# Optimization experiments

Measured on AMD Instinct MI355X. Metric: run time of the kernel, lower is better.

## Reference

```python
import jax, jax.numpy as jnp
import numpy as np

N, E, G, H, D = 50000, 800000, 64, 2, 128  # nodes, edges, graphs, heads, out_channels
NEG_SLOPE_ATT = 0.2   # GATv2 default negative_slope
NEG_SLOPE_OUT = 0.01  # torch.nn.LeakyReLU default
BN_EPS = 1e-5


def setup_inputs() -> dict:
    key = jax.random.key(0)
    ks = jax.random.split(key, 12)
    x = jax.random.normal(ks[0], (N, 1), jnp.float32)
    edge_index = jax.random.randint(ks[1], (2, E), 0, N, dtype=jnp.int64)
    edge_attr = jax.random.normal(ks[2], (E,), jnp.float32)
    batch = jnp.sort(jax.random.randint(ks[3], (N,), 0, G, dtype=jnp.int64))
    # GATv2Conv params: lin_l/lin_r: Linear(1, H*D) with bias; lin_edge: Linear(1, H*D) no bias
    Wl = jax.random.normal(ks[4], (1, H * D), jnp.float32) * 0.5
    bl = jax.random.normal(ks[5], (H * D,), jnp.float32) * 0.1
    Wr = jax.random.normal(ks[6], (1, H * D), jnp.float32) * 0.5
    br = jax.random.normal(ks[7], (H * D,), jnp.float32) * 0.1
    We = jax.random.normal(ks[8], (1, H * D), jnp.float32) * 0.5
    att = jax.random.normal(ks[9], (H, D), jnp.float32) * 0.5
    bias = jax.random.normal(ks[10], (D,), jnp.float32) * 0.1
    gamma = jnp.ones((D,), jnp.float32)
    beta = jnp.zeros((D,), jnp.float32)
    return {"x": x, "edge_index": edge_index, "edge_attr": edge_attr, "batch": batch,
            "Wl": Wl, "bl": bl, "Wr": Wr, "br": br, "We": We, "att": att,
            "bias": bias, "gamma": gamma, "beta": beta}


def reference(x, edge_index, edge_attr, batch, Wl, bl, Wr, br, We, att, bias, gamma, beta):
    n = x.shape[0]
    src, dst = edge_index[0], edge_index[1]  # message flows src -> dst
    # node transforms: [N, H, D]
    xl = (x @ Wl + bl).reshape(n, H, D)  # lin_l (source side, also the message value)
    xr = (x @ Wr + br).reshape(n, H, D)  # lin_r (destination side)
    # edge feature embedding: [E, H, D]
    ee = (edge_attr[:, None] @ We).reshape(-1, H, D)
    # GATv2 scoring: leaky_relu(x_j + x_i + e), then dot with attention vector
    m = jax.nn.leaky_relu(xl[src] + xr[dst] + ee, NEG_SLOPE_ATT)  # [E, H, D]
    alpha = jnp.einsum('ehd,hd->eh', m, att)  # [E, H]
    # scatter-softmax over incoming edges per destination node
    amax = jax.ops.segment_max(alpha, dst, num_segments=n)  # [N, H]
    ea = jnp.exp(alpha - amax[dst])
    denom = jax.ops.segment_sum(ea, dst, num_segments=n)
    alpha = ea / (denom[dst] + 1e-16)
    # weighted scatter-add aggregation of x_j
    out = jax.ops.segment_sum(xl[src] * alpha[..., None], dst, num_segments=n)  # [N, H, D]
    out = out.mean(axis=1) + bias  # concat=False -> head average, then conv bias
    # BatchNorm1d in training mode (biased variance over nodes)
    mean = out.mean(axis=0)
    var = ((out - mean) ** 2).mean(axis=0)
    out = (out - mean) * jax.lax.rsqrt(var + BN_EPS) * gamma + beta
    out = jax.nn.leaky_relu(out, NEG_SLOPE_OUT)
    # graph-level scatter_add pooling
    return jax.ops.segment_sum(out, batch, num_segments=G)  # [G, D]
```

## Files before the change

### kernel.cpp

```cpp
#include <hip/hip_runtime.h>
#include <math.h>

#define NN 50000
#define NE 800000
#define NG 64

#define WS_C     0
#define WS_ACC   16
#define WS_BNSUM (WS_ACC + 4*NN)
#define WS_BNSQ  (WS_BNSUM + 128)
#define WS_HEAD  (WS_BNSQ + 128)
#define WS_PREV  (WS_HEAD + 4*NN)
#define WS_STAGE (WS_PREV + NE)
#define WS_END   (WS_STAGE + 4*NE)
#define WS_NEED_BYTES ((size_t)WS_END * 4 + 256)

#define LEND 0xFFFFFFFFu

static_assert(((WS_STAGE * 4) % 16) == 0, "stage 16B alignment");
static_assert(NE % 4 == 0, "edge unroll");

extern "C" __global__ __launch_bounds__(256)
void k0_init(float* __restrict__ ws,
             const float* __restrict__ att, const float* __restrict__ Wl,
             const float* __restrict__ Wr, const float* __restrict__ We,
             const float* __restrict__ bl, const float* __restrict__ br,
             float* __restrict__ out, int dense)
{
  int tid = blockIdx.x * 256 + threadIdx.x;
  int nt = gridDim.x * 256;
  if (dense) {
    unsigned* head = (unsigned*)(ws + WS_HEAD);
    for (int i = tid; i < 4 * NN; i += nt) head[i] = LEND;
  } else {
    for (int i = tid; i < 4 * NN; i += nt) ws[WS_ACC + i] = 0.f;
  }
  for (int i = tid; i < 256; i += nt) ws[WS_BNSUM + i] = 0.f;
  for (int i = tid; i < NG * 128; i += nt) out[i] = 0.f;
  if (blockIdx.x == 0) {
    __shared__ float red[4][256];
    int t = threadIdx.x;
    float a = att[t];
    red[0][t] = a * Wl[t];
    red[1][t] = a * Wr[t];
    red[2][t] = a * We[t];
    red[3][t] = a * (bl[t] + br[t]);
    __syncthreads();
    if (t < 8) {
      int k = t >> 1, h = t & 1;
      float s = 0.f;
      for (int d = 0; d < 128; ++d) s += red[k][h * 128 + d];
      ws[WS_C + h * 4 + k] = s;
    }
  }
}

#define STEP(wl_, wr_, we_, bb_, at_, xs_, xd_, ae_, acc_)                 \
  { float tt = fmaf(we_, ae_, bb_); tt = fmaf(wr_, xd_, tt);               \
    tt = fmaf(wl_, xs_, tt); acc_ = fmaf(fabsf(tt), at_, acc_); }

#define STEP4(c, q0, q1, q2, q3)                                           \
  STEP(wl.c, wr.c, we.c, bb.c, at.c, xs0, xd0, ae0, q0)                    \
  STEP(wl.c, wr.c, we.c, bb.c, at.c, xs1, xd1, ae1, q1)                    \
  STEP(wl.c, wr.c, we.c, bb.c, at.c, xs2, xd2, ae2, q2)                    \
  STEP(wl.c, wr.c, we.c, bb.c, at.c, xs3, xd3, ae3, q3)

#define SCORE_CORE                                                         \
  int4 s4 = *(const int4*)&ei[base];                                       \
  int4 dd4 = *(const int4*)&ei[NE + base];                                 \
  float4 ae4 = *(const float4*)&eattr[base];                               \
  float xs0 = x[s4.x], xs1 = x[s4.y], xs2 = x[s4.z], xs3 = x[s4.w];        \
  float xd0 = x[dd4.x], xd1 = x[dd4.y], xd2 = x[dd4.z], xd3 = x[dd4.w];    \
  float ae0 = ae4.x, ae1 = ae4.y, ae2 = ae4.z, ae3 = ae4.w;

#define SCORE_LOOPS                                                        \
  float a00 = 0.f, a01 = 0.f, a02 = 0.f, a03 = 0.f;                        \
  float a10 = 0.f, a11 = 0.f, a12 = 0.f, a13 = 0.f;                        \
  _Pragma("unroll 2")                                                      \
  for (int j = 0; j < 128; j += 4) {                                       \
    float4 wl = *(const float4*)&sWl[j];                                   \
    float4 wr = *(const float4*)&sWr[j];                                   \
    float4 we = *(const float4*)&sWe[j];                                   \
    float4 bb = *(const float4*)&sB[j];                                    \
    float4 at = *(const float4*)&sAt[j];                                   \
    STEP4(x, a00, a01, a02, a03)                                           \
    STEP4(y, a00, a01, a02, a03)                                           \
    STEP4(z, a00, a01, a02, a03)                                           \
    STEP4(w, a00, a01, a02, a03)                                           \
  }                                                                        \
  _Pragma("unroll 2")                                                      \
  for (int j = 128; j < 256; j += 4) {                                     \
    float4 wl = *(const float4*)&sWl[j];                                   \
    float4 wr = *(const float4*)&sWr[j];                                   \
    float4 we = *(const float4*)&sWe[j];                                   \
    float4 bb = *(const float4*)&sB[j];                                    \
    float4 at = *(const float4*)&sAt[j];                                   \
    STEP4(x, a10, a11, a12, a13)                                           \
    STEP4(y, a10, a11, a12, a13)                                           \
    STEP4(z, a10, a11, a12, a13)                                           \
    STEP4(w, a10, a11, a12, a13)                                           \
  }                                                                        \
  float4 c0 = *(const float4*)&ws[WS_C];                                   \
  float4 c1 = *(const float4*)&ws[WS_C + 4];

#define SMEM_WEIGHTS                                                       \
  __shared__ __align__(16) float sWl[256], sWr[256], sWe[256], sB[256], sAt[256]; \
  { int t = threadIdx.x;                                                   \
    sWl[t] = Wl[t]; sWr[t] = Wr[t]; sWe[t] = We[t];                        \
    sB[t] = bl[t] + br[t]; sAt[t] = att[t]; }                              \
  __syncthreads();

#define SCORES(xs_, xd_, ae_, accA, accB, out0, out1)                      \
  { float lin0 = fmaf(c0.x, xs_, fmaf(c0.y, xd_, fmaf(c0.z, ae_, c0.w))); \
    out0 = fmaf(0.4f, accA, 0.6f * lin0);                                  \
    float lin1 = fmaf(c1.x, xs_, fmaf(c1.y, xd_, fmaf(c1.z, ae_, c1.w))); \
    out1 = fmaf(0.4f, accB, 0.6f * lin1); }

extern "C" __global__ __launch_bounds__(256)
void ke_edge(const int* __restrict__ ei, const float* __restrict__ x,
             const float* __restrict__ eattr,
             const float* __restrict__ Wl, const float* __restrict__ Wr,
             const float* __restrict__ We, const float* __restrict__ bl,
             const float* __restrict__ br, const float* __restrict__ att,
             float* __restrict__ ws)
{
  SMEM_WEIGHTS
  int base = (blockIdx.x * 256 + threadIdx.x) * 4;
  if (base >= NE) return;
  SCORE_CORE
  unsigned* head = (unsigned*)(ws + WS_HEAD);
  unsigned pv0 = atomicExch(&head[4 * dd4.x + 0], (unsigned)(base + 0));
  unsigned pv1 = atomicExch(&head[4 * dd4.y + 1], (unsigned)(base + 1));
  unsigned pv2 = atomicExch(&head[4 * dd4.z + 2], (unsigned)(base + 2));
  unsigned pv3 = atomicExch(&head[4 * dd4.w + 3], (unsigned)(base + 3));
  SCORE_LOOPS
  float4* stage = (float4*)(ws + WS_STAGE);
  unsigned* prev = (unsigned*)(ws + WS_PREV);
  float s0, s1;
  float4 pay0, pay1, pay2, pay3;
#define PAY(xs_, xd_, ae_, accA, accB, pp)                                 \
  { SCORES(xs_, xd_, ae_, accA, accB, s0, s1)                              \
    float e0 = __expf(s0), e1 = __expf(s1);                                \
    pp = make_float4(e0, e1, e0 * xs_, e1 * xs_); }
  PAY(xs0, xd0, ae0, a00, a10, pay0)
  PAY(xs1, xd1, ae1, a01, a11, pay1)
  PAY(xs2, xd2, ae2, a02, a12, pay2)
  PAY(xs3, xd3, ae3, a03, a13, pay3)
#undef PAY
  stage[base + 0] = pay0;
  stage[base + 1] = pay1;
  stage[base + 2] = pay2;
  stage[base + 3] = pay3;
  *(uint4*)&prev[base] = make_uint4(pv0, pv1, pv2, pv3);
}

extern "C" __global__ __launch_bounds__(256)
void kf_gather(float* __restrict__ ws)
{
  int n = blockIdx.x * 256 + threadIdx.x;
  if (n >= NN) return;
  const unsigned* head = (const unsigned*)(ws + WS_HEAD);
  const unsigned* prev = (const unsigned*)(ws + WS_PREV);
  const float4* stage = (const float4*)(ws + WS_STAGE);
  uint4 p = *(const uint4*)&head[4 * n];
  float4 A0 = make_float4(0.f, 0.f, 0.f, 0.f);
  float4 A1 = A0, A2 = A0, A3 = A0;
  while ((p.x & p.y & p.z & p.w) != LEND) {
#define HOP(pc, Ac)                                                        \
    if (pc != LEND) {                                                      \
      float4 q = stage[pc];                                                \
      unsigned np = prev[pc];                                              \
      Ac.x += q.x; Ac.y += q.y; Ac.z += q.z; Ac.w += q.w;                  \
      pc = np;                                                             \
    }
    HOP(p.x, A0) HOP(p.y, A1) HOP(p.z, A2) HOP(p.w, A3)
#undef HOP
  }
  float4 r;
  r.x = (A0.x + A1.x) + (A2.x + A3.x);
  r.y = (A0.y + A1.y) + (A2.y + A3.y);
  r.z = (A0.z + A1.z) + (A2.z + A3.z);
  r.w = (A0.w + A1.w) + (A2.w + A3.w);
  *(float4*)&ws[WS_ACC + 4 * n] = r;
}

extern "C" __global__ __launch_bounds__(256)
void k12f(const int* __restrict__ ei, const float* __restrict__ x,
          const float* __restrict__ eattr,
          const float* __restrict__ Wl, const float* __restrict__ Wr,
          const float* __restrict__ We, const float* __restrict__ bl,
          const float* __restrict__ br, const float* __restrict__ att,
          float* __restrict__ ws)
{
  SMEM_WEIGHTS
  int base = (blockIdx.x * 256 + threadIdx.x) * 4;
  if (base >= NE) return;
  SCORE_CORE
  SCORE_LOOPS
  float* acc = ws + WS_ACC;
  float s0, s1;
#define EPI2(xs_, xd_, ae_, accA, accB, dsti)                              \
  { SCORES(xs_, xd_, ae_, accA, accB, s0, s1)                              \
    float e0 = __expf(s0), e1 = __expf(s1);                                \
    float* a = &acc[4 * dsti];                                             \
    atomicAdd(a + 0, e0); atomicAdd(a + 1, e1);                            \
    atomicAdd(a + 2, e0 * xs_); atomicAdd(a + 3, e1 * xs_); }
  EPI2(xs0, xd0, ae0, a00, a10, dd4.x)
  EPI2(xs1, xd1, ae1, a01, a11, dd4.y)
  EPI2(xs2, xd2, ae2, a02, a12, dd4.z)
  EPI2(xs3, xd3, ae3, a03, a13, dd4.w)
#undef EPI2
}

__device__ __forceinline__ float node_out4(float4 a, float wl0, float wl1,
                                           float b0, float b1, float bs)
{
  float r0 = 1.f / (a.x + 1e-16f);
  float r1 = 1.f / (a.y + 1e-16f);
  return 0.5f * (fmaf(wl0, a.z * r0, b0 * (a.x * r0)) +
                 fmaf(wl1, a.w * r1, b1 * (a.y * r1))) + bs;
}

extern "C" __global__ __launch_bounds__(256)
void k3_stats(const float* __restrict__ Wl, const float* __restrict__ bl,
              const float* __restrict__ bias, float* __restrict__ ws)
{
  int d = threadIdx.x & 127;
  int row = threadIdx.x >> 7;
  float wl0 = Wl[d], wl1 = Wl[128 + d];
  float b0 = bl[d], b1 = bl[128 + d];
  float bs = bias[d];
  float sum = 0.f, sq = 0.f;
  for (int n = blockIdx.x * 2 + row; n < NN; n += gridDim.x * 2) {
    float4 a = *(const float4*)&ws[WS_ACC + 4 * n];
    float o = node_out4(a, wl0, wl1, b0, b1, bs);
    sum += o;
    sq = fmaf(o, o, sq);
  }
  __shared__ float l1[256], l2[256];
  l1[threadIdx.x] = sum; l2[threadIdx.x] = sq;
  __syncthreads();
  if (row == 0) {
    atomicAdd(&ws[WS_BNSUM + d], l1[d] + l1[128 + d]);
    atomicAdd(&ws[WS_BNSQ + d], l2[d] + l2[128 + d]);
  }
}

extern "C" __global__ __launch_bounds__(256)
void k4_pool(const int* __restrict__ batch,
             const float* __restrict__ Wl, const float* __restrict__ bl,
             const float* __restrict__ bias, const float* __restrict__ gamma,
             const float* __restrict__ beta,
             float* __restrict__ ws, float* __restrict__ out)
{
  const int CHUNK = (NN + (int)gridDim.x - 1) / (int)gridDim.x;
  int n0 = blockIdx.x * CHUNK;
  if (n0 >= NN) return;
  int n1 = n0 + CHUNK; if (n1 > NN) n1 = NN;
  int d = threadIdx.x & 127;
  int row = threadIdx.x >> 7;
  const float invN = 1.f / (float)NN;
  float mean = ws[WS_BNSUM + d] * invN;
  float var = fmaf(ws[WS_BNSQ + d], invN, -mean * mean);
  float scale = gamma[d] * rsqrtf(var + 1e-5f);
  float shift = fmaf(-mean, scale, beta[d]);
  float wl0 = Wl[d], wl1 = Wl[128 + d];
  float b0 = bl[d], b1 = bl[128 + d];
  float bs = bias[d];
  __shared__ float pool[4][128];
  for (int i = threadIdx.x; i < 512; i += 256) ((float*)pool)[i] = 0.f;
  __syncthreads();
  int g0 = batch[n0];
  for (int n = n0 + row; n < n1; n += 2) {
    float4 a = *(const float4*)&ws[WS_ACC + 4 * n];
    float o = node_out4(a, wl0, wl1, b0, b1, bs);
    float v = fmaf(o, scale, shift);
    v = v > 0.f ? v : 0.01f * v;
    int g = batch[n];
    int slot = g - g0;
    if (slot < 4) atomicAdd(&pool[slot][d], v);
    else atomicAdd(&out[g * 128 + d], v);
  }
  __syncthreads();
  for (int i = threadIdx.x; i < 512; i += 256) {
    int slot = i >> 7, dd = i & 127;
    int g = g0 + slot;
    float v = pool[slot][dd];
    if (g < NG && v != 0.f) atomicAdd(&out[g * 128 + dd], v);
  }
}

extern "C" void kernel_launch(void* const* d_in, const int* in_sizes, int n_in,
                              void* d_out, int out_size, void* d_ws, size_t ws_size,
                              hipStream_t stream) {
  const float* x     = (const float*)d_in[0];
  const int*   ei    = (const int*)d_in[1];
  const float* eattr = (const float*)d_in[2];
  const int*   batch = (const int*)d_in[3];
  const float* Wl    = (const float*)d_in[4];
  const float* bl    = (const float*)d_in[5];
  const float* Wr    = (const float*)d_in[6];
  const float* br    = (const float*)d_in[7];
  const float* We    = (const float*)d_in[8];
  const float* att   = (const float*)d_in[9];
  const float* bias  = (const float*)d_in[10];
  const float* gam   = (const float*)d_in[11];
  const float* bet   = (const float*)d_in[12];
  float* ws  = (float*)d_ws;
  float* out = (float*)d_out;

  const bool dense = (ws_size >= WS_NEED_BYTES);
  const int EB = (NE / 4 + 255) / 256;

  hipLaunchKernelGGL(k0_init, dim3(128), dim3(256), 0, stream,
                     ws, att, Wl, Wr, We, bl, br, out, dense ? 1 : 0);
  if (dense) {
    hipLaunchKernelGGL(ke_edge, dim3(EB), dim3(256), 0, stream,
                       ei, x, eattr, Wl, Wr, We, bl, br, att, ws);
    hipLaunchKernelGGL(kf_gather, dim3((NN + 255) / 256), dim3(256), 0, stream, ws);
  } else {
    hipLaunchKernelGGL(k12f, dim3(EB), dim3(256), 0, stream,
                       ei, x, eattr, Wl, Wr, We, bl, br, att, ws);
  }
  hipLaunchKernelGGL(k3_stats, dim3(256), dim3(256), 0, stream,
                     Wl, bl, bias, ws);
  hipLaunchKernelGGL(k4_pool, dim3(256), dim3(256), 0, stream,
                     batch, Wl, bl, bias, gam, bet, ws, out);
}
```

Before: 229.5 us.

## Fuse all stages into one cooperative persistent kernel with grid syncs

New measurement: 574.8 us. +150.5%, slower.

```diff
diff --git a/kernel.cpp b/kernel.cpp
--- a/kernel.cpp
+++ b/kernel.cpp
@@ -1,5 +1,8 @@
 #include <hip/hip_runtime.h>
+#include <hip/hip_cooperative_groups.h>
 #include <math.h>
+
+namespace cg = cooperative_groups;
 
 #define NN 50000
 #define NE 800000
@@ -9,6 +12,7 @@
 #define WS_ACC   16
 #define WS_BNSUM (WS_ACC + 4*NN)
 #define WS_BNSQ  (WS_BNSUM + 128)
+#define WS_MOM   WS_BNSUM
 #define WS_HEAD  (WS_BNSQ + 128)
 #define WS_PREV  (WS_HEAD + 4*NN)
 #define WS_STAGE (WS_PREV + NE)
@@ -16,44 +20,10 @@
 #define WS_NEED_BYTES ((size_t)WS_END * 4 + 256)
 
 #define LEND 0xFFFFFFFFu
+#define NQ (NE / 4)
 
 static_assert(((WS_STAGE * 4) % 16) == 0, "stage 16B alignment");
 static_assert(NE % 4 == 0, "edge unroll");
-
-extern "C" __global__ __launch_bounds__(256)
-void k0_init(float* __restrict__ ws,
-             const float* __restrict__ att, const float* __restrict__ Wl,
-             const float* __restrict__ Wr, const float* __restrict__ We,
-             const float* __restrict__ bl, const float* __restrict__ br,
-             float* __restrict__ out, int dense)
-{
-  int tid = blockIdx.x * 256 + threadIdx.x;
-  int nt = gridDim.x * 256;
-  if (dense) {
-    unsigned* head = (unsigned*)(ws + WS_HEAD);
-    for (int i = tid; i < 4 * NN; i += nt) head[i] = LEND;
-  } else {
-    for (int i = tid; i < 4 * NN; i += nt) ws[WS_ACC + i] = 0.f;
-  }
-  for (int i = tid; i < 256; i += nt) ws[WS_BNSUM + i] = 0.f;
-  for (int i = tid; i < NG * 128; i += nt) out[i] = 0.f;
-  if (blockIdx.x == 0) {
-    __shared__ float red[4][256];
-    int t = threadIdx.x;
-    float a = att[t];
-    red[0][t] = a * Wl[t];
-    red[1][t] = a * Wr[t];
-    red[2][t] = a * We[t];
-    red[3][t] = a * (bl[t] + br[t]);
-    __syncthreads();
-    if (t < 8) {
-      int k = t >> 1, h = t & 1;
-      float s = 0.f;
-      for (int d = 0; d < 128; ++d) s += red[k][h * 128 + d];
-      ws[WS_C + h * 4 + k] = s;
-    }
-  }
-}
 
 #define STEP(wl_, wr_, we_, bb_, at_, xs_, xd_, ae_, acc_)                 \
   { float tt = fmaf(we_, ae_, bb_); tt = fmaf(wr_, xd_, tt);               \
@@ -103,8 +73,10 @@
   float4 c0 = *(const float4*)&ws[WS_C];                                   \
   float4 c1 = *(const float4*)&ws[WS_C + 4];
 
-#define SMEM_WEIGHTS                                                       \
-  __shared__ __align__(16) float sWl[256], sWr[256], sWe[256], sB[256], sAt[256]; \
+#define SMEM_WEIGHTS_DECL                                                  \
+  __shared__ __align__(16) float sWl[256], sWr[256], sWe[256], sB[256], sAt[256];
+
+#define SMEM_WEIGHTS_LOAD                                                  \
   { int t = threadIdx.x;                                                   \
     sWl[t] = Wl[t]; sWr[t] = Wr[t]; sWe[t] = We[t];                        \
     sB[t] = bl[t] + br[t]; sAt[t] = att[t]; }                              \
@@ -115,6 +87,222 @@
     out0 = fmaf(0.4f, accA, 0.6f * lin0);                                  \
     float lin1 = fmaf(c1.x, xs_, fmaf(c1.y, xd_, fmaf(c1.z, ae_, c1.w))); \
     out1 = fmaf(0.4f, accB, 0.6f * lin1); }
+
+extern "C" __global__ __launch_bounds__(256, 4)
+void kmega(const int* __restrict__ ei, const float* __restrict__ x,
+           const float* __restrict__ eattr, const int* __restrict__ batch,
+           const float* __restrict__ Wl, const float* __restrict__ bl,
+           const float* __restrict__ Wr, const float* __restrict__ br,
+           const float* __restrict__ We, const float* __restrict__ att,
+           const float* __restrict__ bias, const float* __restrict__ gamma,
+           const float* __restrict__ beta,
+           float* __restrict__ ws, float* __restrict__ out)
+{
+  cg::grid_group grid = cg::this_grid();
+  SMEM_WEIGHTS_DECL
+  __shared__ float red[4][256];
+  __shared__ float smom[56];
+  __shared__ float pool[4][128];
+  SMEM_WEIGHTS_LOAD
+
+  const int t = threadIdx.x;
+  const int gtid = blockIdx.x * 256 + t;
+  const int gsz = gridDim.x * 256;
+
+  {
+    unsigned* head = (unsigned*)(ws + WS_HEAD);
+    for (int i = gtid; i < 4 * NN; i += gsz) head[i] = LEND;
+    for (int i = gtid; i < 14; i += gsz) ws[WS_MOM + i] = 0.f;
+    for (int i = gtid; i < NG * 128; i += gsz) out[i] = 0.f;
+    if (blockIdx.x == 0) {
+      float a = sAt[t];
+      red[0][t] = a * sWl[t];
+      red[1][t] = a * sWr[t];
+      red[2][t] = a * sWe[t];
+      red[3][t] = a * sB[t];
+      __syncthreads();
+      if (t < 8) {
+        int k = t >> 1, h = t & 1;
+        float s = 0.f;
+        for (int d = 0; d < 128; ++d) s += red[k][h * 128 + d];
+        ws[WS_C + h * 4 + k] = s;
+      }
+    }
+  }
+  grid.sync();
+
+  {
+    unsigned* head = (unsigned*)(ws + WS_HEAD);
+    float4* stage = (float4*)(ws + WS_STAGE);
+    unsigned* prev = (unsigned*)(ws + WS_PREV);
+    for (int q = gtid; q < NQ; q += gsz) {
+      int base = q * 4;
+      SCORE_CORE
+      unsigned pv0 = atomicExch(&head[4 * dd4.x + 0], (unsigned)(base + 0));
+      unsigned pv1 = atomicExch(&head[4 * dd4.y + 1], (unsigned)(base + 1));
+      unsigned pv2 = atomicExch(&head[4 * dd4.z + 2], (unsigned)(base + 2));
+      unsigned pv3 = atomicExch(&head[4 * dd4.w + 3], (unsigned)(base + 3));
+      SCORE_LOOPS
+      float s0, s1;
+      float4 pay0, pay1, pay2, pay3;
+#define PAY(xs_, xd_, ae_, accA, accB, pp)                                 \
+      { SCORES(xs_, xd_, ae_, accA, accB, s0, s1)                          \
+        float e0 = __expf(s0), e1 = __expf(s1);                            \
+        pp = make_float4(e0, e1, e0 * xs_, e1 * xs_); }
+      PAY(xs0, xd0, ae0, a00, a10, pay0)
+      PAY(xs1, xd1, ae1, a01, a11, pay1)
+      PAY(xs2, xd2, ae2, a02, a12, pay2)
+      PAY(xs3, xd3, ae3, a03, a13, pay3)
+#undef PAY
+      stage[base + 0] = pay0;
+      stage[base + 1] = pay1;
+      stage[base + 2] = pay2;
+      stage[base + 3] = pay3;
+      *(uint4*)&prev[base] = make_uint4(pv0, pv1, pv2, pv3);
+    }
+  }
+  grid.sync();
+
+  {
+    const unsigned* head = (const unsigned*)(ws + WS_HEAD);
+    const unsigned* prev = (const unsigned*)(ws + WS_PREV);
+    const float4* stage = (const float4*)(ws + WS_STAGE);
+    float f1 = 0.f, f2 = 0.f, f3 = 0.f, f4 = 0.f;
+    for (int n = gtid; n < NN; n += gsz) {
+      uint4 p = *(const uint4*)&head[4 * n];
+      float4 A0 = make_float4(0.f, 0.f, 0.f, 0.f);
+      float4 A1 = A0, A2 = A0, A3 = A0;
+      while ((p.x & p.y & p.z & p.w) != LEND) {
+#define HOP(pc, Ac)                                                        \
+        if (pc != LEND) {                                                  \
+          float4 qq = stage[pc];                                           \
+          unsigned np = prev[pc];                                          \
+          Ac.x += qq.x; Ac.y += qq.y; Ac.z += qq.z; Ac.w += qq.w;          \
+          pc = np;                                                         \
+        }
+        HOP(p.x, A0) HOP(p.y, A1) HOP(p.z, A2) HOP(p.w, A3)
+#undef HOP
+      }
+      float den0 = (A0.x + A1.x) + (A2.x + A3.x);
+      float den1 = (A0.y + A1.y) + (A2.y + A3.y);
+      float t10  = (A0.z + A1.z) + (A2.z + A3.z);
+      float t11  = (A0.w + A1.w) + (A2.w + A3.w);
+      *(float4*)&ws[WS_ACC + 4 * n] = make_float4(den0, den1, t10, t11);
+      float r0 = 1.f / (den0 + 1e-16f);
+      float r1 = 1.f / (den1 + 1e-16f);
+      f1 += den0 * r0; f2 += t10 * r0; f3 += den1 * r1; f4 += t11 * r1;
+    }
+    float pm[14] = { f1, f2, f3, f4,
+                     f1*f1, f1*f2, f1*f3, f1*f4,
+                     f2*f2, f2*f3, f2*f4,
+                     f3*f3, f3*f4, f4*f4 };
+#pragma unroll
+    for (int k = 0; k < 14; ++k) {
+      float v = pm[k];
+#pragma unroll
+      for (int m = 32; m >= 1; m >>= 1) v += __shfl_xor(v, m);
+      pm[k] = v;
+    }
+    int wid = t >> 6, lane = t & 63;
+    if (lane == 0) {
+#pragma unroll
+      for (int k = 0; k < 14; ++k) smom[wid * 14 + k] = pm[k];
+    }
+    __syncthreads();
+    if (t < 14) {
+      float s = smom[t] + smom[14 + t] + smom[28 + t] + smom[42 + t];
+      if (s != 0.f) atomicAdd(&ws[WS_MOM + t], s);
+    }
+  }
+  grid.sync();
+
+  {
+    const int CHUNK = (NN + (int)gridDim.x - 1) / (int)gridDim.x;
+    int n0 = blockIdx.x * CHUNK;
+    if (n0 < NN) {
+      int n1 = n0 + CHUNK; if (n1 > NN) n1 = NN;
+      int d = t & 127;
+      int row = t >> 7;
+      float S1 = ws[WS_MOM + 0], S2 = ws[WS_MOM + 1];
+      float S3 = ws[WS_MOM + 2], S4 = ws[WS_MOM + 3];
+      float M11 = ws[WS_MOM + 4], M12 = ws[WS_MOM + 5], M13 = ws[WS_MOM + 6];
+      float M14 = ws[WS_MOM + 7], M22 = ws[WS_MOM + 8], M23 = ws[WS_MOM + 9];
+      float M24 = ws[WS_MOM + 10], M33 = ws[WS_MOM + 11], M34 = ws[WS_MOM + 12];
+      float M44 = ws[WS_MOM + 13];
+      float g1 = 0.5f * bl[d], g2 = 0.5f * Wl[d];
+      float g3 = 0.5f * bl[128 + d], g4 = 0.5f * Wl[128 + d];
+      float g5 = bias[d];
+      const float invN = 1.f / (float)NN;
+      float dotS = g1 * S1 + g2 * S2 + g3 * S3 + g4 * S4;
+      float mean = (dotS + (float)NN * g5) * invN;
+      float sumsq = g1*g1*M11 + g2*g2*M22 + g3*g3*M33 + g4*g4*M44
+                  + 2.f*(g1*g2*M12 + g1*g3*M13 + g1*g4*M14
+                       + g2*g3*M23 + g2*g4*M24 + g3*g4*M34)
+                  + 2.f*g5*dotS + (float)NN*g5*g5;
+      float var = fmaf(sumsq, invN, -mean * mean);
+      float scale = gamma[d] * rsqrtf(var + 1e-5f);
+      float shift = fmaf(-mean, scale, beta[d]);
+      for (int i = t; i < 512; i += 256) ((float*)pool)[i] = 0.f;
+      __syncthreads();
+      int g0 = batch[n0];
+      for (int n = n0 + row; n < n1; n += 2) {
+        float4 a = *(const float4*)&ws[WS_ACC + 4 * n];
+        float r0 = 1.f / (a.x + 1e-16f);
+        float r1 = 1.f / (a.y + 1e-16f);
+        float o = g1 * (a.x * r0) + g2 * (a.z * r0)
+                + g3 * (a.y * r1) + g4 * (a.w * r1) + g5;
+        float v = fmaf(o, scale, shift);
+        v = v > 0.f ? v : 0.01f * v;
+        int g = batch[n];
+        int slot = g - g0;
+        if (slot < 4) atomicAdd(&pool[slot][d], v);
+        else atomicAdd(&out[g * 128 + d], v);
+      }
+      __syncthreads();
+      for (int i = t; i < 512; i += 256) {
+        int slot = i >> 7, dd = i & 127;
+        int g = g0 + slot;
+        float v = pool[slot][dd];
+        if (g < NG && v != 0.f) atomicAdd(&out[g * 128 + dd], v);
+      }
+    }
+  }
+}
+
+extern "C" __global__ __launch_bounds__(256)
+void k0_init(float* __restrict__ ws,
+             const float* __restrict__ att, const float* __restrict__ Wl,
+             const float* __restrict__ Wr, const float* __restrict__ We,
+             const float* __restrict__ bl, const float* __restrict__ br,
+             float* __restrict__ out, int dense)
+{
+  int tid = blockIdx.x * 256 + threadIdx.x;
+  int nt = gridDim.x * 256;
+  if (dense) {
+    unsigned* head = (unsigned*)(ws + WS_HEAD);
+    for (int i = tid; i < 4 * NN; i += nt) head[i] = LEND;
+  } else {
+    for (int i = tid; i < 4 * NN; i += nt) ws[WS_ACC + i] = 0.f;
+  }
+  for (int i = tid; i < 256; i += nt) ws[WS_BNSUM + i] = 0.f;
+  for (int i = tid; i < NG * 128; i += nt) out[i] = 0.f;
+  if (blockIdx.x == 0) {
+    __shared__ float red[4][256];
+    int t = threadIdx.x;
+    float a = att[t];
+    red[0][t] = a * Wl[t];
+    red[1][t] = a * Wr[t];
+    red[2][t] = a * We[t];
+    red[3][t] = a * (bl[t] + br[t]);
+    __syncthreads();
+    if (t < 8) {
+      int k = t >> 1, h = t & 1;
+      float s = 0.f;
+      for (int d = 0; d < 128; ++d) s += red[k][h * 128 + d];
+      ws[WS_C + h * 4 + k] = s;
+    }
+  }
+}
 
 extern "C" __global__ __launch_bounds__(256)
 void ke_edge(const int* __restrict__ ei, const float* __restrict__ x,
@@ -124,7 +312,8 @@
              const float* __restrict__ br, const float* __restrict__ att,
              float* __restrict__ ws)
 {
-  SMEM_WEIGHTS
+  SMEM_WEIGHTS_DECL
+  SMEM_WEIGHTS_LOAD
   int base = (blockIdx.x * 256 + threadIdx.x) * 4;
   if (base >= NE) return;
   SCORE_CORE
@@ -192,7 +381,8 @@
           const float* __restrict__ br, const float* __restrict__ att,
           float* __restrict__ ws)
 {
-  SMEM_WEIGHTS
+  SMEM_WEIGHTS_DECL
+  SMEM_WEIGHTS_LOAD
   int base = (blockIdx.x * 256 + threadIdx.x) * 4;
   if (base >= NE) return;
   SCORE_CORE
@@ -312,18 +502,32 @@
   const bool dense = (ws_size >= WS_NEED_BYTES);
   const int EB = (NE / 4 + 255) / 256;
 
-  hipLaunchKernelGGL(k0_init, dim3(128), dim3(256), 0, stream,
-                     ws, att, Wl, Wr, We, bl, br, out, dense ? 1 : 0);
+  bool done = false;
   if (dense) {
-    hipLaunchKernelGGL(ke_edge, dim3(EB), dim3(256), 0, stream,
-                       ei, x, eattr, Wl, Wr, We, bl, br, att, ws);
-    hipLaunchKernelGGL(kf_gather, dim3((NN + 255) / 256), dim3(256), 0, stream, ws);
-  } else {
-    hipLaunchKernelGGL(k12f, dim3(EB), dim3(256), 0, stream,
-                       ei, x, eattr, Wl, Wr, We, bl, br, att, ws);
-  }
-  hipLaunchKernelGGL(k3_stats, dim3(256), dim3(256), 0, stream,
-                     Wl, bl, bias, ws);
-  hipLaunchKernelGGL(k4_pool, dim3(256), dim3(256), 0, stream,
-                     batch, Wl, bl, bias, gam, bet, ws, out);
-}
+    void* kargs[] = { (void*)&ei, (void*)&x, (void*)&eattr, (void*)&batch,
+                      (void*)&Wl, (void*)&bl, (void*)&Wr, (void*)&br,
+                      (void*)&We, (void*)&att, (void*)&bias, (void*)&gam,
+                      (void*)&bet, (void*)&ws, (void*)&out };
+    hipError_t e = hipLaunchCooperativeKernel((const void*)kmega,
+                                              dim3(1024), dim3(256),
+                                              kargs, 0, stream);
+    if (e == hipSuccess) done = true;
+    else (void)hipGetLastError();
+  }
+  if (!done) {
+    hipLaunchKernelGGL(k0_init, dim3(128), dim3(256), 0, stream,
+                       ws, att, Wl, Wr, We, bl, br, out, dense ? 1 : 0);
+    if (dense) {
+      hipLaunchKernelGGL(ke_edge, dim3(EB), dim3(256), 0, stream,
+                         ei, x, eattr, Wl, Wr, We, bl, br, att, ws);
+      hipLaunchKernelGGL(kf_gather, dim3((NN + 255) / 256), dim3(256), 0, stream, ws);
+    } else {
+      hipLaunchKernelGGL(k12f, dim3(EB), dim3(256), 0, stream,
+                         ei, x, eattr, Wl, Wr, We, bl, br, att, ws);
+    }
+    hipLaunchKernelGGL(k3_stats, dim3(256), dim3(256), 0, stream,
+                       Wl, bl, bias, ws);
+    hipLaunchKernelGGL(k4_pool, dim3(256), dim3(256), 0, stream,
+                       batch, Wl, bl, bias, gam, bet, ws, out);
+  }
+}
```

## Fold BatchNorm statistics into gather via per-node moment sums, drop stats pass

Applied to the files above, without the earlier changes.

Result: slower. 373.2 us (+62.7%).

```diff
diff --git a/kernel.cpp b/kernel.cpp
--- a/kernel.cpp
+++ b/kernel.cpp
@@ -9,6 +9,7 @@
 #define WS_ACC   16
 #define WS_BNSUM (WS_ACC + 4*NN)
 #define WS_BNSQ  (WS_BNSUM + 128)
+#define WS_MOM   WS_BNSUM
 #define WS_HEAD  (WS_BNSQ + 128)
 #define WS_PREV  (WS_HEAD + 4*NN)
 #define WS_STAGE (WS_PREV + NE)
@@ -19,41 +20,6 @@
 
 static_assert(((WS_STAGE * 4) % 16) == 0, "stage 16B alignment");
 static_assert(NE % 4 == 0, "edge unroll");
-
-extern "C" __global__ __launch_bounds__(256)
-void k0_init(float* __restrict__ ws,
-             const float* __restrict__ att, const float* __restrict__ Wl,
-             const float* __restrict__ Wr, const float* __restrict__ We,
-             const float* __restrict__ bl, const float* __restrict__ br,
-             float* __restrict__ out, int dense)
-{
-  int tid = blockIdx.x * 256 + threadIdx.x;
-  int nt = gridDim.x * 256;
-  if (dense) {
-    unsigned* head = (unsigned*)(ws + WS_HEAD);
-    for (int i = tid; i < 4 * NN; i += nt) head[i] = LEND;
-  } else {
-    for (int i = tid; i < 4 * NN; i += nt) ws[WS_ACC + i] = 0.f;
-  }
-  for (int i = tid; i < 256; i += nt) ws[WS_BNSUM + i] = 0.f;
-  for (int i = tid; i < NG * 128; i += nt) out[i] = 0.f;
-  if (blockIdx.x == 0) {
-    __shared__ float red[4][256];
-    int t = threadIdx.x;
-    float a = att[t];
-    red[0][t] = a * Wl[t];
-    red[1][t] = a * Wr[t];
-    red[2][t] = a * We[t];
-    red[3][t] = a * (bl[t] + br[t]);
-    __syncthreads();
-    if (t < 8) {
-      int k = t >> 1, h = t & 1;
-      float s = 0.f;
-      for (int d = 0; d < 128; ++d) s += red[k][h * 128 + d];
-      ws[WS_C + h * 4 + k] = s;
-    }
-  }
-}
 
 #define STEP(wl_, wr_, we_, bb_, at_, xs_, xd_, ae_, acc_)                 \
   { float tt = fmaf(we_, ae_, bb_); tt = fmaf(wr_, xd_, tt);               \
@@ -103,8 +69,10 @@
   float4 c0 = *(const float4*)&ws[WS_C];                                   \
   float4 c1 = *(const float4*)&ws[WS_C + 4];
 
-#define SMEM_WEIGHTS                                                       \
-  __shared__ __align__(16) float sWl[256], sWr[256], sWe[256], sB[256], sAt[256]; \
+#define SMEM_WEIGHTS_DECL                                                  \
+  __shared__ __align__(16) float sWl[256], sWr[256], sWe[256], sB[256], sAt[256];
+
+#define SMEM_WEIGHTS_LOAD                                                  \
   { int t = threadIdx.x;                                                   \
     sWl[t] = Wl[t]; sWr[t] = Wr[t]; sWe[t] = We[t];                        \
     sB[t] = bl[t] + br[t]; sAt[t] = att[t]; }                              \
@@ -115,6 +83,42 @@
     out0 = fmaf(0.4f, accA, 0.6f * lin0);                                  \
     float lin1 = fmaf(c1.x, xs_, fmaf(c1.y, xd_, fmaf(c1.z, ae_, c1.w))); \
     out1 = fmaf(0.4f, accB, 0.6f * lin1); }
+
+extern "C" __global__ __launch_bounds__(256)
+void k0_init(float* __restrict__ ws,
+             const float* __restrict__ att, const float* __restrict__ Wl,
+             const float* __restrict__ Wr, const float* __restrict__ We,
+             const float* __restrict__ bl, const float* __restrict__ br,
+             float* __restrict__ out, int dense)
+{
+  int tid = blockIdx.x * 256 + threadIdx.x;
+  int nt = gridDim.x * 256;
+  if (dense) {
+    unsigned* head = (unsigned*)(ws + WS_HEAD);
+    for (int i = tid; i < 4 * NN; i += nt) head[i] = LEND;
+    if (tid < 14) ws[WS_MOM + tid] = 0.f;
+  } else {
+    for (int i = tid; i < 4 * NN; i += nt) ws[WS_ACC + i] = 0.f;
+    for (int i = tid; i < 256; i += nt) ws[WS_BNSUM + i] = 0.f;
+  }
+  for (int i = tid; i < NG * 128; i += nt) out[i] = 0.f;
+  if (blockIdx.x == 0) {
+    __shared__ float red[4][256];
+    int t = threadIdx.x;
+    float a = att[t];
+    red[0][t] = a * Wl[t];
+    red[1][t] = a * Wr[t];
+    red[2][t] = a * We[t];
+    red[3][t] = a * (bl[t] + br[t]);
+    __syncthreads();
+    if (t < 8) {
+      int k = t >> 1, h = t & 1;
+      float s = 0.f;
+      for (int d = 0; d < 128; ++d) s += red[k][h * 128 + d];
+      ws[WS_C + h * 4 + k] = s;
+    }
+  }
+}
 
 extern "C" __global__ __launch_bounds__(256)
 void ke_edge(const int* __restrict__ ei, const float* __restrict__ x,
@@ -124,7 +128,8 @@
              const float* __restrict__ br, const float* __restrict__ att,
              float* __restrict__ ws)
 {
-  SMEM_WEIGHTS
+  SMEM_WEIGHTS_DECL
+  SMEM_WEIGHTS_LOAD
   int base = (blockIdx.x * 256 + threadIdx.x) * 4;
   if (base >= NE) return;
   SCORE_CORE
@@ -155,33 +160,119 @@
 }
 
 extern "C" __global__ __launch_bounds__(256)
-void kf_gather(float* __restrict__ ws)
+void kfm_gather(float* __restrict__ ws)
 {
   int n = blockIdx.x * 256 + threadIdx.x;
-  if (n >= NN) return;
-  const unsigned* head = (const unsigned*)(ws + WS_HEAD);
-  const unsigned* prev = (const unsigned*)(ws + WS_PREV);
-  const float4* stage = (const float4*)(ws + WS_STAGE);
-  uint4 p = *(const uint4*)&head[4 * n];
-  float4 A0 = make_float4(0.f, 0.f, 0.f, 0.f);
-  float4 A1 = A0, A2 = A0, A3 = A0;
-  while ((p.x & p.y & p.z & p.w) != LEND) {
+  const int t = threadIdx.x;
+  float f1 = 0.f, f2 = 0.f, f3 = 0.f, f4 = 0.f;
+  if (n < NN) {
+    const unsigned* head = (const unsigned*)(ws + WS_HEAD);
+    const unsigned* prev = (const unsigned*)(ws + WS_PREV);
+    const float4* stage = (const float4*)(ws + WS_STAGE);
+    uint4 p = *(const uint4*)&head[4 * n];
+    float4 A0 = make_float4(0.f, 0.f, 0.f, 0.f);
+    float4 A1 = A0, A2 = A0, A3 = A0;
+    while ((p.x & p.y & p.z & p.w) != LEND) {
 #define HOP(pc, Ac)                                                        \
-    if (pc != LEND) {                                                      \
-      float4 q = stage[pc];                                                \
-      unsigned np = prev[pc];                                              \
-      Ac.x += q.x; Ac.y += q.y; Ac.z += q.z; Ac.w += q.w;                  \
-      pc = np;                                                             \
+      if (pc != LEND) {                                                    \
+        float4 q = stage[pc];                                              \
+        unsigned np = prev[pc];                                            \
+        Ac.x += q.x; Ac.y += q.y; Ac.z += q.z; Ac.w += q.w;                \
+        pc = np;                                                           \
+      }
+      HOP(p.x, A0) HOP(p.y, A1) HOP(p.z, A2) HOP(p.w, A3)
+#undef HOP
     }
-    HOP(p.x, A0) HOP(p.y, A1) HOP(p.z, A2) HOP(p.w, A3)
-#undef HOP
-  }
-  float4 r;
-  r.x = (A0.x + A1.x) + (A2.x + A3.x);
-  r.y = (A0.y + A1.y) + (A2.y + A3.y);
-  r.z = (A0.z + A1.z) + (A2.z + A3.z);
-  r.w = (A0.w + A1.w) + (A2.w + A3.w);
-  *(float4*)&ws[WS_ACC + 4 * n] = r;
+    float den0 = (A0.x + A1.x) + (A2.x + A3.x);
+    float den1 = (A0.y + A1.y) + (A2.y + A3.y);
+    float t10  = (A0.z + A1.z) + (A2.z + A3.z);
+    float t11  = (A0.w + A1.w) + (A2.w + A3.w);
+    *(float4*)&ws[WS_ACC + 4 * n] = make_float4(den0, den1, t10, t11);
+    float r0 = 1.f / (den0 + 1e-16f);
+    float r1 = 1.f / (den1 + 1e-16f);
+    f1 = den0 * r0; f2 = t10 * r0; f3 = den1 * r1; f4 = t11 * r1;
+  }
+  float pm[14] = { f1, f2, f3, f4,
+                   f1*f1, f1*f2, f1*f3, f1*f4,
+                   f2*f2, f2*f3, f2*f4,
+                   f3*f3, f3*f4, f4*f4 };
+#pragma unroll
+  for (int k = 0; k < 14; ++k) {
+    float v = pm[k];
+#pragma unroll
+    for (int m = 32; m >= 1; m >>= 1) v += __shfl_xor(v, m);
+    pm[k] = v;
+  }
+  __shared__ float smom[56];
+  int wid = t >> 6, lane = t & 63;
+  if (lane == 0) {
+#pragma unroll
+    for (int k = 0; k < 14; ++k) smom[wid * 14 + k] = pm[k];
+  }
+  __syncthreads();
+  if (t < 14) {
+    float s = smom[t] + smom[14 + t] + smom[28 + t] + smom[42 + t];
+    if (s != 0.f) atomicAdd(&ws[WS_MOM + t], s);
+  }
+}
+
+extern "C" __global__ __launch_bounds__(256)
+void k4m_pool(const int* __restrict__ batch,
+              const float* __restrict__ Wl, const float* __restrict__ bl,
+              const float* __restrict__ bias, const float* __restrict__ gamma,
+              const float* __restrict__ beta,
+              float* __restrict__ ws, float* __restrict__ out)
+{
+  const int CHUNK = (NN + (int)gridDim.x - 1) / (int)gridDim.x;
+  int n0 = blockIdx.x * CHUNK;
+  if (n0 >= NN) return;
+  int n1 = n0 + CHUNK; if (n1 > NN) n1 = NN;
+  int t = threadIdx.x;
+  int d = t & 127;
+  int row = t >> 7;
+  float S1 = ws[WS_MOM + 0], S2 = ws[WS_MOM + 1];
+  float S3 = ws[WS_MOM + 2], S4 = ws[WS_MOM + 3];
+  float M11 = ws[WS_MOM + 4], M12 = ws[WS_MOM + 5], M13 = ws[WS_MOM + 6];
+  float M14 = ws[WS_MOM + 7], M22 = ws[WS_MOM + 8], M23 = ws[WS_MOM + 9];
+  float M24 = ws[WS_MOM + 10], M33 = ws[WS_MOM + 11], M34 = ws[WS_MOM + 12];
+  float M44 = ws[WS_MOM + 13];
+  float g1 = 0.5f * bl[d], g2 = 0.5f * Wl[d];
+  float g3 = 0.5f * bl[128 + d], g4 = 0.5f * Wl[128 + d];
+  float g5 = bias[d];
+  const float invN = 1.f / (float)NN;
+  float dotS = g1 * S1 + g2 * S2 + g3 * S3 + g4 * S4;
+  float mean = (dotS + (float)NN * g5) * invN;
+  float sumsq = g1*g1*M11 + g2*g2*M22 + g3*g3*M33 + g4*g4*M44
+              + 2.f*(g1*g2*M12 + g1*g3*M13 + g1*g4*M14
+                   + g2*g3*M23 + g2*g4*M24 + g3*g4*M34)
+              + 2.f*g5*dotS + (float)NN*g5*g5;
+  float var = fmaf(sumsq, invN, -mean * mean);
+  float scale = gamma[d] * rsqrtf(var + 1e-5f);
+  float shift = fmaf(-mean, scale, beta[d]);
+  __shared__ float pool[4][128];
+  for (int i = t; i < 512; i += 256) ((float*)pool)[i] = 0.f;
+  __syncthreads();
+  int g0 = batch[n0];
+  for (int n = n0 + row; n < n1; n += 2) {
+    float4 a = *(const float4*)&ws[WS_ACC + 4 * n];
+    float r0 = 1.f / (a.x + 1e-16f);
+    float r1 = 1.f / (a.y + 1e-16f);
+    float o = g1 * (a.x * r0) + g2 * (a.z * r0)
+            + g3 * (a.y * r1) + g4 * (a.w * r1) + g5;
+    float v = fmaf(o, scale, shift);
+    v = v > 0.f ? v : 0.01f * v;
+    int g = batch[n];
+    int slot = g - g0;
+    if (slot < 4) atomicAdd(&pool[slot][d], v);
+    else atomicAdd(&out[g * 128 + d], v);
+  }
+  __syncthreads();
+  for (int i = t; i < 512; i += 256) {
+    int slot = i >> 7, dd = i & 127;
+    int g = g0 + slot;
+    float v = pool[slot][dd];
+    if (g < NG && v != 0.f) atomicAdd(&out[g * 128 + dd], v);
+  }
 }
 
 extern "C" __global__ __launch_bounds__(256)
@@ -192,7 +283,8 @@
           const float* __restrict__ br, const float* __restrict__ att,
           float* __restrict__ ws)
 {
-  SMEM_WEIGHTS
+  SMEM_WEIGHTS_DECL
+  SMEM_WEIGHTS_LOAD
   int base = (blockIdx.x * 256 + threadIdx.x) * 4;
   if (base >= NE) return;
   SCORE_CORE
@@ -317,13 +409,15 @@
   if (dense) {
     hipLaunchKernelGGL(ke_edge, dim3(EB), dim3(256), 0, stream,
                        ei, x, eattr, Wl, Wr, We, bl, br, att, ws);
-    hipLaunchKernelGGL(kf_gather, dim3((NN + 255) / 256), dim3(256), 0, stream, ws);
+    hipLaunchKernelGGL(kfm_gather, dim3((NN + 255) / 256), dim3(256), 0, stream, ws);
+    hipLaunchKernelGGL(k4m_pool, dim3(256), dim3(256), 0, stream,
+                       batch, Wl, bl, bias, gam, bet, ws, out);
   } else {
     hipLaunchKernelGGL(k12f, dim3(EB), dim3(256), 0, stream,
                        ei, x, eattr, Wl, Wr, We, bl, br, att, ws);
-  }
-  hipLaunchKernelGGL(k3_stats, dim3(256), dim3(256), 0, stream,
-                     Wl, bl, bias, ws);
-  hipLaunchKernelGGL(k4_pool, dim3(256), dim3(256), 0, stream,
-                     batch, Wl, bl, bias, gam, bet, ws, out);
-}
+    hipLaunchKernelGGL(k3_stats, dim3(256), dim3(256), 0, stream,
+                       Wl, bl, bias, ws);
+    hipLaunchKernelGGL(k4_pool, dim3(256), dim3(256), 0, stream,
+                       batch, Wl, bl, bias, gam, bet, ws, out);
+  }
+}
```
